# Performance work log

Measured on AMD Instinct MI355X. Metric: run time of the kernel, lower is better.

## Reference

```python
import jax, jax.numpy as jnp
import numpy as np

NUM_NODES_PLUS_EDGES = 850000
NUM_EDGES = 800000
HIDDEN = 128


def setup_inputs() -> dict:
    key = jax.random.key(0)
    k1, k2, k3, k4, k5 = jax.random.split(key, 5)
    node_edge_feat = jax.random.normal(k1, (NUM_NODES_PLUS_EDGES, HIDDEN), dtype=jnp.float32)
    dist_feat = jax.random.normal(k2, (NUM_EDGES, HIDDEN), dtype=jnp.float32)
    srcs = jax.random.randint(k3, (NUM_EDGES,), 0, NUM_NODES_PLUS_EDGES, dtype=jnp.int64)
    dsts = jax.random.randint(k4, (NUM_EDGES,), 0, NUM_NODES_PLUS_EDGES, dtype=jnp.int64)
    # fc: Linear(3*hidden -> hidden); W stored as [in, out] for x @ W + b
    W = jax.random.normal(k5, (3 * HIDDEN, HIDDEN), dtype=jnp.float32) * (1.0 / np.sqrt(3 * HIDDEN))
    b = jnp.zeros((HIDDEN,), dtype=jnp.float32)
    return {"node_edge_feat": node_edge_feat, "dist_feat": dist_feat,
            "srcs": srcs, "dsts": dsts, "W": W, "b": b}


def reference(node_edge_feat, dist_feat, srcs, dsts, W, b):
    # gather src/dst features: [num_edges, hidden] each
    src_feat = node_edge_feat[srcs]
    dst_feat = node_edge_feat[dsts]
    # split weight so we avoid materializing the concat explicitly
    W_src, W_dst, W_dist = W[:HIDDEN], W[HIDDEN:2 * HIDDEN], W[2 * HIDDEN:]
    h = src_feat @ W_src + dst_feat @ W_dst + dist_feat @ W_dist + b
    return jax.nn.relu(h)
```

## Files before the change

### kernel.cpp

```cpp
#include <hip/hip_runtime.h>
#include <hip/hip_bf16.h>

#define HIDDEN 128
#define NEDGES 800000
#define TILE_M 32
#define KDIM 384
#define NKSTEP 12
#define NTILES (NEDGES / TILE_M)

typedef __attribute__((ext_vector_type(8))) short short8;
typedef __attribute__((ext_vector_type(4))) float f32x4;

__device__ __forceinline__ unsigned short f2bf(float x) {
    union { __hip_bfloat16 b; unsigned short u; } c;
    c.b = __float2bfloat16(x);
    return c.u;
}

__global__ void __launch_bounds__(256) pack_w_kernel(const float* __restrict__ W,
                                                     unsigned short* __restrict__ Wp) {
    int t = blockIdx.x * 256 + threadIdx.x;
    if (t >= 96 * 64) return;
    int lane = t & 63;
    int frag = t >> 6;
    int ks = frag >> 3, nf = frag & 7;
    int hi = lane >> 4, lo = lane & 15;
    short8 g;
#pragma unroll
    for (int i = 0; i < 8; ++i) {
        int k = ks * 32 + hi * 8 + i;
        int n = nf * 16 + lo;
        g[i] = (short)f2bf(W[k * HIDDEN + n]);
    }
    *(short8*)(Wp + (size_t)t * 8) = g;
}

#define CVT8(ldsrow_, u_, v_, col8_, swz_)                                   \
    do {                                                                     \
        short8 pk;                                                           \
        pk[0] = (short)f2bf((u_).x); pk[1] = (short)f2bf((u_).y);            \
        pk[2] = (short)f2bf((u_).z); pk[3] = (short)f2bf((u_).w);            \
        pk[4] = (short)f2bf((v_).x); pk[5] = (short)f2bf((v_).y);            \
        pk[6] = (short)f2bf((v_).z); pk[7] = (short)f2bf((v_).w);            \
        *(short8*)((ldsrow_) + (size_t)(((col8_) ^ (swz_)) * 8)) = pk;       \
    } while (0)

__global__ void __launch_bounds__(256, 2) edge_gemm_kernel(
    const float* __restrict__ nef,
    const float* __restrict__ dist,
    const int*   __restrict__ srcs,
    const int*   __restrict__ dsts,
    const unsigned short* __restrict__ Wp,
    const float* __restrict__ bias,
    float*       __restrict__ out)
{
    __shared__ __align__(16) unsigned short A_lds[TILE_M * KDIM];

    const int tid  = threadIdx.x;
    const int lane = tid & 63;
    const int wid  = tid >> 6;
    const int lo   = lane & 15;
    const int hi   = lane >> 4;

    const float bv0 = bias[wid * 32 + lo];
    const float bv1 = bias[wid * 32 + 16 + lo];

    const int eg  = tid >> 3;
    const int lt  = tid & 7;
    const int swz = eg & 7;
    unsigned short* ldsrow = A_lds + eg * KDIM;

    const unsigned short* wbase = Wp + ((size_t)(wid * 2) * 64 + lane) * 8;

    int tile = blockIdx.x;
    const int stride = gridDim.x;
    if (tile >= NTILES) return;

    int e0 = tile * TILE_M + eg;
    int s_cur = srcs[e0], d_cur = dsts[e0];
    int s_nxt = 0, d_nxt = 0;
    {
        int t1 = tile + stride;
        if (t1 < NTILES) { int e1 = t1 * TILE_M + eg; s_nxt = srcs[e1]; d_nxt = dsts[e1]; }
    }

    float4 r0, r1, r2, r3, r4, r5, r6, r7, r8, r9, r10, r11;
    {
        const float4* srow = (const float4*)nef  + (size_t)s_cur * 32;
        const float4* drow = (const float4*)nef  + (size_t)d_cur * 32;
        const float4* frow = (const float4*)dist + (size_t)e0 * 32;
        const int g0 = 2 * lt, g1 = 2 * (lt + 8);
        r0 = srow[g0]; r1 = srow[g0 + 1]; r2 = srow[g1]; r3 = srow[g1 + 1];
        r4 = drow[g0]; r5 = drow[g0 + 1]; r6 = drow[g1]; r7 = drow[g1 + 1];
        r8 = frow[g0]; r9 = frow[g0 + 1]; r10 = frow[g1]; r11 = frow[g1 + 1];
    }

    while (tile < NTILES) {
        CVT8(ldsrow, r0, r1, lt,          swz);
        CVT8(ldsrow, r2, r3, lt + 8,      swz);
        CVT8(ldsrow, r4, r5, 16 + lt,     swz);
        CVT8(ldsrow, r6, r7, 16 + lt + 8, swz);
        CVT8(ldsrow, r8, r9, 32 + lt,     swz);
        CVT8(ldsrow, r10, r11, 32 + lt + 8, swz);
        __syncthreads();

        const int t_next = tile + stride;
        if (t_next < NTILES) {
            int en = t_next * TILE_M + eg;
            const float4* srow = (const float4*)nef  + (size_t)s_nxt * 32;
            const float4* drow = (const float4*)nef  + (size_t)d_nxt * 32;
            const float4* frow = (const float4*)dist + (size_t)en * 32;
            const int g0 = 2 * lt, g1 = 2 * (lt + 8);
            r0 = srow[g0]; r1 = srow[g0 + 1]; r2 = srow[g1]; r3 = srow[g1 + 1];
            r4 = drow[g0]; r5 = drow[g0 + 1]; r6 = drow[g1]; r7 = drow[g1 + 1];
            r8 = frow[g0]; r9 = frow[g0 + 1]; r10 = frow[g1]; r11 = frow[g1 + 1];
            int t2 = t_next + stride;
            if (t2 < NTILES) { int e2 = t2 * TILE_M + eg; s_nxt = srcs[e2]; d_nxt = dsts[e2]; }
        }

        f32x4 acc00 = {0.f, 0.f, 0.f, 0.f};
        f32x4 acc01 = {0.f, 0.f, 0.f, 0.f};
        f32x4 acc10 = {0.f, 0.f, 0.f, 0.f};
        f32x4 acc11 = {0.f, 0.f, 0.f, 0.f};
#pragma unroll
        for (int ks = 0; ks < NKSTEP; ++ks) {
            short8 b0 = *(const short8*)(wbase + (size_t)(ks * 8) * 512);
            short8 b1 = *(const short8*)(wbase + (size_t)(ks * 8 + 1) * 512);
            const int c8 = ks * 4 + hi;
            short8 a0 = *(const short8*)(A_lds + lo * KDIM + ((c8 ^ (lo & 7)) * 8));
            short8 a1 = *(const short8*)(A_lds + (16 + lo) * KDIM + ((c8 ^ (lo & 7)) * 8));
            acc00 = __builtin_amdgcn_mfma_f32_16x16x32_bf16(a0, b0, acc00, 0, 0, 0);
            acc01 = __builtin_amdgcn_mfma_f32_16x16x32_bf16(a0, b1, acc01, 0, 0, 0);
            acc10 = __builtin_amdgcn_mfma_f32_16x16x32_bf16(a1, b0, acc10, 0, 0, 0);
            acc11 = __builtin_amdgcn_mfma_f32_16x16x32_bf16(a1, b1, acc11, 0, 0, 0);
        }
        __syncthreads();

#pragma unroll
        for (int rr = 0; rr < 4; ++rr) {
            const int row0 = tile * TILE_M + hi * 4 + rr;
            const int row1 = row0 + 16;
            const int col0 = wid * 32 + lo;
            const int col1 = col0 + 16;
            float v00 = acc00[rr] + bv0;
            float v01 = acc01[rr] + bv1;
            float v10 = acc10[rr] + bv0;
            float v11 = acc11[rr] + bv1;
            out[(size_t)row0 * HIDDEN + col0] = v00 > 0.f ? v00 : 0.f;
            out[(size_t)row0 * HIDDEN + col1] = v01 > 0.f ? v01 : 0.f;
            out[(size_t)row1 * HIDDEN + col0] = v10 > 0.f ? v10 : 0.f;
            out[(size_t)row1 * HIDDEN + col1] = v11 > 0.f ? v11 : 0.f;
        }

        tile = t_next;
    }
}

extern "C" void kernel_launch(void* const* d_in, const int* in_sizes, int n_in,
                              void* d_out, int out_size, void* d_ws, size_t ws_size,
                              hipStream_t stream) {
    const float* nef  = (const float*)d_in[0];
    const float* dist = (const float*)d_in[1];
    const int*   srcs = (const int*)d_in[2];
    const int*   dsts = (const int*)d_in[3];
    const float* W    = (const float*)d_in[4];
    const float* bias = (const float*)d_in[5];
    float* out = (float*)d_out;
    unsigned short* Wp = (unsigned short*)d_ws;

    hipLaunchKernelGGL(pack_w_kernel, dim3(24), dim3(256), 0, stream, W, Wp);
    hipLaunchKernelGGL(edge_gemm_kernel, dim3(1024), dim3(256), 0, stream,
                       nef, dist, srcs, dsts, Wp, bias, out);
}
```

Measured before the change: 278.4 us.

## Double-buffer LDS tile, hold weight fragments in registers, add nontemporal streaming

Each wave now loads its slice of the packed weight fragments into registers once, before the loop, so the per-k-step global weight loads are gone. The A tile in LDS is double-buffered, which removes the second barrier per tile. Streaming dist loads and output stores use nontemporal hints, and the grid is halved to 512 blocks. Holding 24 short8 weight fragments in registers costs many VGPRs and may reduce occupancy, and halving the grid lowers parallelism.

```diff
diff --git a/kernel.cpp b/kernel.cpp
--- a/kernel.cpp
+++ b/kernel.cpp
@@ -10,6 +10,7 @@
 
 typedef __attribute__((ext_vector_type(8))) short short8;
 typedef __attribute__((ext_vector_type(4))) float f32x4;
+typedef __attribute__((ext_vector_type(4))) float f4;
 
 __device__ __forceinline__ unsigned short f2bf(float x) {
     union { __hip_bfloat16 b; unsigned short u; } c;
@@ -38,10 +39,10 @@
 #define CVT8(ldsrow_, u_, v_, col8_, swz_)                                   \
     do {                                                                     \
         short8 pk;                                                           \
-        pk[0] = (short)f2bf((u_).x); pk[1] = (short)f2bf((u_).y);            \
-        pk[2] = (short)f2bf((u_).z); pk[3] = (short)f2bf((u_).w);            \
-        pk[4] = (short)f2bf((v_).x); pk[5] = (short)f2bf((v_).y);            \
-        pk[6] = (short)f2bf((v_).z); pk[7] = (short)f2bf((v_).w);            \
+        pk[0] = (short)f2bf((u_)[0]); pk[1] = (short)f2bf((u_)[1]);          \
+        pk[2] = (short)f2bf((u_)[2]); pk[3] = (short)f2bf((u_)[3]);          \
+        pk[4] = (short)f2bf((v_)[0]); pk[5] = (short)f2bf((v_)[1]);          \
+        pk[6] = (short)f2bf((v_)[2]); pk[7] = (short)f2bf((v_)[3]);          \
         *(short8*)((ldsrow_) + (size_t)(((col8_) ^ (swz_)) * 8)) = pk;       \
     } while (0)
 
@@ -54,7 +55,7 @@
     const float* __restrict__ bias,
     float*       __restrict__ out)
 {
-    __shared__ __align__(16) unsigned short A_lds[TILE_M * KDIM];
+    __shared__ __align__(16) unsigned short A_lds[2][TILE_M * KDIM];
 
     const int tid  = threadIdx.x;
     const int lane = tid & 63;
@@ -68,9 +69,16 @@
     const int eg  = tid >> 3;
     const int lt  = tid & 7;
     const int swz = eg & 7;
-    unsigned short* ldsrow = A_lds + eg * KDIM;
 
-    const unsigned short* wbase = Wp + ((size_t)(wid * 2) * 64 + lane) * 8;
+    short8 bfrag[NKSTEP][2];
+#pragma unroll
+    for (int ks = 0; ks < NKSTEP; ++ks) {
+#pragma unroll
+        for (int nf = 0; nf < 2; ++nf) {
+            int frag = ks * 8 + wid * 2 + nf;
+            bfrag[ks][nf] = *(const short8*)(Wp + ((size_t)frag * 64 + lane) * 8);
+        }
+    }
 
     int tile = blockIdx.x;
     const int stride = gridDim.x;
@@ -84,36 +92,45 @@
         if (t1 < NTILES) { int e1 = t1 * TILE_M + eg; s_nxt = srcs[e1]; d_nxt = dsts[e1]; }
     }
 
-    float4 r0, r1, r2, r3, r4, r5, r6, r7, r8, r9, r10, r11;
+    f4 r0, r1, r2, r3, r4, r5, r6, r7, r8, r9, r10, r11;
     {
-        const float4* srow = (const float4*)nef  + (size_t)s_cur * 32;
-        const float4* drow = (const float4*)nef  + (size_t)d_cur * 32;
-        const float4* frow = (const float4*)dist + (size_t)e0 * 32;
+        const f4* srow = (const f4*)nef  + (size_t)s_cur * 32;
+        const f4* drow = (const f4*)nef  + (size_t)d_cur * 32;
+        const f4* frow = (const f4*)dist + (size_t)e0 * 32;
         const int g0 = 2 * lt, g1 = 2 * (lt + 8);
         r0 = srow[g0]; r1 = srow[g0 + 1]; r2 = srow[g1]; r3 = srow[g1 + 1];
         r4 = drow[g0]; r5 = drow[g0 + 1]; r6 = drow[g1]; r7 = drow[g1 + 1];
-        r8 = frow[g0]; r9 = frow[g0 + 1]; r10 = frow[g1]; r11 = frow[g1 + 1];
+        r8  = __builtin_nontemporal_load(frow + g0);
+        r9  = __builtin_nontemporal_load(frow + g0 + 1);
+        r10 = __builtin_nontemporal_load(frow + g1);
+        r11 = __builtin_nontemporal_load(frow + g1 + 1);
     }
 
+    int p = 0;
     while (tile < NTILES) {
-        CVT8(ldsrow, r0, r1, lt,          swz);
-        CVT8(ldsrow, r2, r3, lt + 8,      swz);
-        CVT8(ldsrow, r4, r5, 16 + lt,     swz);
-        CVT8(ldsrow, r6, r7, 16 + lt + 8, swz);
-        CVT8(ldsrow, r8, r9, 32 + lt,     swz);
+        unsigned short* ldsrow = A_lds[p] + eg * KDIM;
+        CVT8(ldsrow, r0, r1, lt,            swz);
+        CVT8(ldsrow, r2, r3, lt + 8,        swz);
+        CVT8(ldsrow, r4, r5, 16 + lt,       swz);
+        CVT8(ldsrow, r6, r7, 16 + lt + 8,   swz);
+        CVT8(ldsrow, r8, r9, 32 + lt,       swz);
         CVT8(ldsrow, r10, r11, 32 + lt + 8, swz);
+
         __syncthreads();
 
         const int t_next = tile + stride;
         if (t_next < NTILES) {
             int en = t_next * TILE_M + eg;
-            const float4* srow = (const float4*)nef  + (size_t)s_nxt * 32;
-            const float4* drow = (const float4*)nef  + (size_t)d_nxt * 32;
-            const float4* frow = (const float4*)dist + (size_t)en * 32;
+            const f4* srow = (const f4*)nef  + (size_t)s_nxt * 32;
+            const f4* drow = (const f4*)nef  + (size_t)d_nxt * 32;
+            const f4* frow = (const f4*)dist + (size_t)en * 32;
             const int g0 = 2 * lt, g1 = 2 * (lt + 8);
             r0 = srow[g0]; r1 = srow[g0 + 1]; r2 = srow[g1]; r3 = srow[g1 + 1];
             r4 = drow[g0]; r5 = drow[g0 + 1]; r6 = drow[g1]; r7 = drow[g1 + 1];
-            r8 = frow[g0]; r9 = frow[g0 + 1]; r10 = frow[g1]; r11 = frow[g1 + 1];
+            r8  = __builtin_nontemporal_load(frow + g0);
+            r9  = __builtin_nontemporal_load(frow + g0 + 1);
+            r10 = __builtin_nontemporal_load(frow + g1);
+            r11 = __builtin_nontemporal_load(frow + g1 + 1);
             int t2 = t_next + stride;
             if (t2 < NTILES) { int e2 = t2 * TILE_M + eg; s_nxt = srcs[e2]; d_nxt = dsts[e2]; }
         }
@@ -122,19 +139,17 @@
         f32x4 acc01 = {0.f, 0.f, 0.f, 0.f};
         f32x4 acc10 = {0.f, 0.f, 0.f, 0.f};
         f32x4 acc11 = {0.f, 0.f, 0.f, 0.f};
+        const unsigned short* abase = A_lds[p];
 #pragma unroll
         for (int ks = 0; ks < NKSTEP; ++ks) {
-            short8 b0 = *(const short8*)(wbase + (size_t)(ks * 8) * 512);
-            short8 b1 = *(const short8*)(wbase + (size_t)(ks * 8 + 1) * 512);
             const int c8 = ks * 4 + hi;
-            short8 a0 = *(const short8*)(A_lds + lo * KDIM + ((c8 ^ (lo & 7)) * 8));
-            short8 a1 = *(const short8*)(A_lds + (16 + lo) * KDIM + ((c8 ^ (lo & 7)) * 8));
-            acc00 = __builtin_amdgcn_mfma_f32_16x16x32_bf16(a0, b0, acc00, 0, 0, 0);
-            acc01 = __builtin_amdgcn_mfma_f32_16x16x32_bf16(a0, b1, acc01, 0, 0, 0);
-            acc10 = __builtin_amdgcn_mfma_f32_16x16x32_bf16(a1, b0, acc10, 0, 0, 0);
-            acc11 = __builtin_amdgcn_mfma_f32_16x16x32_bf16(a1, b1, acc11, 0, 0, 0);
+            short8 a0 = *(const short8*)(abase + lo * KDIM + ((c8 ^ (lo & 7)) * 8));
+            short8 a1 = *(const short8*)(abase + (16 + lo) * KDIM + ((c8 ^ (lo & 7)) * 8));
+            acc00 = __builtin_amdgcn_mfma_f32_16x16x32_bf16(a0, bfrag[ks][0], acc00, 0, 0, 0);
+            acc01 = __builtin_amdgcn_mfma_f32_16x16x32_bf16(a0, bfrag[ks][1], acc01, 0, 0, 0);
+            acc10 = __builtin_amdgcn_mfma_f32_16x16x32_bf16(a1, bfrag[ks][0], acc10, 0, 0, 0);
+            acc11 = __builtin_amdgcn_mfma_f32_16x16x32_bf16(a1, bfrag[ks][1], acc11, 0, 0, 0);
         }
-        __syncthreads();
 
 #pragma unroll
         for (int rr = 0; rr < 4; ++rr) {
@@ -146,13 +161,14 @@
             float v01 = acc01[rr] + bv1;
             float v10 = acc10[rr] + bv0;
             float v11 = acc11[rr] + bv1;
-            out[(size_t)row0 * HIDDEN + col0] = v00 > 0.f ? v00 : 0.f;
-            out[(size_t)row0 * HIDDEN + col1] = v01 > 0.f ? v01 : 0.f;
-            out[(size_t)row1 * HIDDEN + col0] = v10 > 0.f ? v10 : 0.f;
-            out[(size_t)row1 * HIDDEN + col1] = v11 > 0.f ? v11 : 0.f;
+            __builtin_nontemporal_store(v00 > 0.f ? v00 : 0.f, &out[(size_t)row0 * HIDDEN + col0]);
+            __builtin_nontemporal_store(v01 > 0.f ? v01 : 0.f, &out[(size_t)row0 * HIDDEN + col1]);
+            __builtin_nontemporal_store(v10 > 0.f ? v10 : 0.f, &out[(size_t)row1 * HIDDEN + col0]);
+            __builtin_nontemporal_store(v11 > 0.f ? v11 : 0.f, &out[(size_t)row1 * HIDDEN + col1]);
         }
 
         tile = t_next;
+        p ^= 1;
     }
 }
 
@@ -169,6 +185,6 @@
     unsigned short* Wp = (unsigned short*)d_ws;
 
     hipLaunchKernelGGL(pack_w_kernel, dim3(24), dim3(256), 0, stream, W, Wp);
-    hipLaunchKernelGGL(edge_gemm_kernel, dim3(1024), dim3(256), 0, stream,
+    hipLaunchKernelGGL(edge_gemm_kernel, dim3(512), dim3(256), 0, stream,
                        nef, dist, srcs, dsts, Wp, bias, out);
 }
```

Measured after the change: 247.3 us. 11.2% less time.
